# Performance work log

Hardware: AMD Instinct MI355X
Metric: run time of the kernel (lower is better)

Reference implementation:

```python
import jax, jax.numpy as jnp
import numpy as np

B, T, N_STOCKS = 256, 250, 500
HIDDEN, N_LAYERS = 512, 2
LB, UB = 0.0, 0.1
N_ITER = 30  # rebalance fixed-point iterations; extra iters are exact no-ops once converged


def setup_inputs() -> dict:
    key = jax.random.key(0)
    ks = jax.random.split(key, 16)
    s = 1.0 / np.sqrt(HIDDEN)  # torch GRU init scale
    inp = {"x": jax.random.normal(ks[0], (B, T, N_STOCKS), jnp.float32)}
    in_dims = [N_STOCKS, HIDDEN]
    for l in range(N_LAYERS):
        inp[f"w_ih_l{l}"] = jax.random.uniform(ks[1 + 4 * l], (3 * HIDDEN, in_dims[l]), jnp.float32, -s, s)
        inp[f"w_hh_l{l}"] = jax.random.uniform(ks[2 + 4 * l], (3 * HIDDEN, HIDDEN), jnp.float32, -s, s)
        inp[f"b_ih_l{l}"] = jax.random.uniform(ks[3 + 4 * l], (3 * HIDDEN,), jnp.float32, -s, s)
        inp[f"b_hh_l{l}"] = jax.random.uniform(ks[4 + 4 * l], (3 * HIDDEN,), jnp.float32, -s, s)
    inp["fc_w"] = jax.random.uniform(ks[9], (N_STOCKS, HIDDEN), jnp.float32, -s, s)
    inp["fc_b"] = jax.random.uniform(ks[10], (N_STOCKS,), jnp.float32, -s, s)
    return inp


def gru_layer(x, w_ih, w_hh, b_ih, b_hh):
    # x: [B, T, D] -> hidden sequence [B, T, H]; torch gate order: r, z, n
    gi = jnp.einsum('btd,gd->btg', x, w_ih) + b_ih  # precompute input gates [B, T, 3H]

    def cell(h, gi_t):
        gh = h @ w_hh.T + b_hh
        i_r, i_z, i_n = jnp.split(gi_t, 3, axis=-1)
        h_r, h_z, h_n = jnp.split(gh, 3, axis=-1)
        r = jax.nn.sigmoid(i_r + h_r)
        z = jax.nn.sigmoid(i_z + h_z)
        n = jnp.tanh(i_n + r * h_n)
        h_new = (1.0 - z) * n + z * h
        return h_new, h_new

    h0 = jnp.zeros((x.shape[0], HIDDEN), x.dtype)
    _, hs = jax.lax.scan(cell, h0, jnp.swapaxes(gi, 0, 1))  # scan over time
    return jnp.swapaxes(hs, 0, 1)


def rebalance(w):
    # Batched capped-simplex redistribution: clamp to [LB, UB], then push the
    # clipped mass onto non-capped entries proportionally; repeat to fixed point.
    def body(w, _):
        wc = jnp.clip(w, LB, UB)
        leftover = jnp.sum(w - wc, axis=-1, keepdims=True)
        nom = jnp.where(wc != UB, wc, 0.0)
        w_new = wc + leftover * nom / jnp.sum(nom, axis=-1, keepdims=True)
        return w_new, None

    w, _ = jax.lax.scan(body, w, None, length=N_ITER)
    return w


def reference(x, w_ih_l0, w_hh_l0, b_ih_l0, b_hh_l0,
              w_ih_l1, w_hh_l1, b_ih_l1, b_hh_l1, fc_w, fc_b):
    h = gru_layer(x, w_ih_l0, w_hh_l0, b_ih_l0, b_hh_l0)
    h = gru_layer(h, w_ih_l1, w_hh_l1, b_ih_l1, b_hh_l1)
    h_t = h[:, -1, :]                      # last timestep [B, H]
    logit = h_t @ fc_w.T + fc_b            # dropout is identity at inference
    logit = jax.nn.silu(logit)             # swish
    w = jax.nn.softmax(logit, axis=-1)
    return rebalance(w)
```

## Files before the change

### kernel.cpp

```cpp
#include <hip/hip_runtime.h>
#include <math.h>

typedef __attribute__((ext_vector_type(8))) short short8;
typedef __attribute__((ext_vector_type(4))) float floatx4;
typedef unsigned short ushort_t;
typedef unsigned int uint32;
typedef unsigned long long u64;

#define BB 256
#define TT 250
#define NS 500
#define HH 512
#define NBLK 256
#define TBLK 256
#define PL_USH 131072u
#define CH_USH 8192u
#define WHI_USH 32768
#define SCR_OFF 131072
#define SMEMB (131072 + 2 * 32 * 65 * 4)

__device__ __forceinline__ ushort_t f2bf(float f) {
    uint32 u = __float_as_uint(f);
    u += 0x7fffu + ((u >> 16) & 1u);
    return (ushort_t)(u >> 16);
}
__device__ __forceinline__ float bf2f(ushort_t h) { return __uint_as_float(((uint32)h) << 16); }
__device__ __forceinline__ float sigm(float x) { return 1.f / (1.f + expf(-x)); }
__device__ __forceinline__ floatx4 mfma16(short8 a, short8 b, floatx4 c) {
    return __builtin_amdgcn_mfma_f32_16x16x32_bf16(a, b, c, 0, 0, 0);
}
__device__ __forceinline__ u64 pack4(const ushort_t* a) {
    return (u64)a[0] | ((u64)a[1] << 16) | ((u64)a[2] << 32) | ((u64)a[3] << 48);
}
__device__ __forceinline__ void st_agent_u32(ushort_t* p, uint32 v) {
    __hip_atomic_store((uint32*)p, v, __ATOMIC_RELAXED, __HIP_MEMORY_SCOPE_AGENT);
}
__device__ __forceinline__ void st_agent_u64(ushort_t* p, u64 v) {
    __hip_atomic_store((u64*)p, v, __ATOMIC_RELAXED, __HIP_MEMORY_SCOPE_AGENT);
}

__device__ __forceinline__ void dbar(unsigned* flags, unsigned phase, int bid) {
    const int tj = threadIdx.x;
    const unsigned v0 = phase << 1, v1 = (phase << 1) | 1u;
    __syncthreads();
    if (tj == 0)
        __hip_atomic_store(flags + ((size_t)bid << 4), v0,
                           __ATOMIC_RELAXED, __HIP_MEMORY_SCOPE_AGENT);
    if (tj >= 1 && tj < 16) {
        unsigned* sp = flags + ((size_t)((bid - tj) & 255) << 4);
        while (__hip_atomic_load(sp, __ATOMIC_RELAXED, __HIP_MEMORY_SCOPE_AGENT) < v0)
            __builtin_amdgcn_s_sleep(2);
    }
    __syncthreads();
    if (tj == 0)
        __hip_atomic_store(flags + ((size_t)bid << 4), v1,
                           __ATOMIC_RELAXED, __HIP_MEMORY_SCOPE_AGENT);
    if (tj >= 1 && tj < 16) {
        unsigned* sp = flags + ((size_t)((bid - (tj << 4)) & 255) << 4);
        while (__hip_atomic_load(sp, __ATOMIC_RELAXED, __HIP_MEMORY_SCOPE_AGENT) < v1)
            __builtin_amdgcn_s_sleep(2);
    }
    __syncthreads();
}

__device__ __forceinline__ float block_max4(float v, float* scr) {
#pragma unroll
    for (int off = 32; off; off >>= 1) v = fmaxf(v, __shfl_down(v, off, 64));
    if ((threadIdx.x & 63) == 0) scr[threadIdx.x >> 6] = v;
    __syncthreads();
    if (threadIdx.x == 0)
        scr[8] = fmaxf(fmaxf(scr[0], scr[1]), fmaxf(scr[2], scr[3]));
    __syncthreads();
    float r = scr[8];
    __syncthreads();
    return r;
}
__device__ __forceinline__ float2 block_sum2_4(float a, float b, float* scr) {
#pragma unroll
    for (int off = 32; off; off >>= 1) {
        a += __shfl_down(a, off, 64);
        b += __shfl_down(b, off, 64);
    }
    if ((threadIdx.x & 63) == 0) { int w = threadIdx.x >> 6; scr[w] = a; scr[4 + w] = b; }
    __syncthreads();
    if (threadIdx.x == 0) {
        scr[8] = scr[0] + scr[1] + scr[2] + scr[3];
        scr[9] = scr[4] + scr[5] + scr[6] + scr[7];
    }
    __syncthreads();
    float2 r = make_float2(scr[8], scr[9]);
    __syncthreads();
    return r;
}

__device__ __forceinline__ void gemm_both(const ushort_t* __restrict__ gp,
                                          const ushort_t* __restrict__ hp,
                                          const ushort_t* whiS, const ushort_t* wloS,
                                          floatx4 (&aGI)[2][2], floatx4 (&aGH)[2][2]) {
    short8 Bh0[8], Bh1[8], Bl0[8], Bl1[8];
    const ushort_t* gpl = gp + PL_USH;
    const ushort_t* hpl = hp + PL_USH;

#define ISSUE(pc) do {                                                                    \
        const ushort_t* _ph = ((pc) < 16) ? (gp + (size_t)(pc) * CH_USH)                  \
                                          : (hp + (size_t)((pc) - 16) * CH_USH);          \
        const ushort_t* _pl = ((pc) < 16) ? (gpl + (size_t)(pc) * CH_USH)                 \
                                          : (hpl + (size_t)((pc) - 16) * CH_USH);         \
        asm volatile("global_load_dwordx4 %0, %1, off sc0 sc1"                            \
                     : "=v"(Bh0[(pc) & 7]) : "v"(_ph));                                   \
        asm volatile("global_load_dwordx4 %0, %1, off offset:1024 sc0 sc1"                \
                     : "=v"(Bh1[(pc) & 7]) : "v"(_ph));                                   \
        asm volatile("global_load_dwordx4 %0, %1, off sc0 sc1"                            \
                     : "=v"(Bl0[(pc) & 7]) : "v"(_pl));                                   \
        asm volatile("global_load_dwordx4 %0, %1, off offset:1024 sc0 sc1"                \
                     : "=v"(Bl1[(pc) & 7]) : "v"(_pl));                                   \
    } while (0)

    ISSUE(0); ISSUE(1); ISSUE(2); ISSUE(3); ISSUE(4); ISSUE(5); ISSUE(6);

    short8 w0h = *(const short8*)(whiS);
    short8 w1h = *(const short8*)(whiS + 512);
    short8 w0l = *(const short8*)(wloS);
    short8 w1l = *(const short8*)(wloS + 512);

#define GSTEP(c, N) do {                                                                  \
        if ((c) + 7 < 32) ISSUE((c) + 7);                                                 \
        short8 n0h, n1h, n0l, n1l;                                                        \
        if ((c) + 1 < 32) {                                                               \
            const size_t _w = (size_t)(((c) + 1) * 2) * 512;                              \
            n0h = *(const short8*)(whiS + _w);                                            \
            n1h = *(const short8*)(whiS + _w + 512);                                      \
            n0l = *(const short8*)(wloS + _w);                                            \
            n1l = *(const short8*)(wloS + _w + 512);                                      \
        }                                                                                 \
        asm volatile("s_waitcnt vmcnt(" #N ")" ::: "memory");                             \
        __builtin_amdgcn_sched_barrier(0);                                                \
        const int _cs = (c) & 7;                                                          \
        floatx4 (&A)[2][2] = ((c) < 16) ? aGI : aGH;                                      \
        A[0][0] = mfma16(w0h, Bh0[_cs], A[0][0]);                                         \
        A[0][1] = mfma16(w0h, Bh1[_cs], A[0][1]);                                         \
        A[1][0] = mfma16(w1h, Bh0[_cs], A[1][0]);                                         \
        A[1][1] = mfma16(w1h, Bh1[_cs], A[1][1]);                                         \
        A[0][0] = mfma16(w0h, Bl0[_cs], A[0][0]);                                         \
        A[0][1] = mfma16(w0h, Bl1[_cs], A[0][1]);                                         \
        A[1][0] = mfma16(w1h, Bl0[_cs], A[1][0]);                                         \
        A[1][1] = mfma16(w1h, Bl1[_cs], A[1][1]);                                         \
        A[0][0] = mfma16(w0l, Bh0[_cs], A[0][0]);                                         \
        A[0][1] = mfma16(w0l, Bh1[_cs], A[0][1]);                                         \
        A[1][0] = mfma16(w1l, Bh0[_cs], A[1][0]);                                         \
        A[1][1] = mfma16(w1l, Bh1[_cs], A[1][1]);                                         \
        if ((c) + 1 < 32) { w0h = n0h; w1h = n1h; w0l = n0l; w1l = n1l; }                 \
    } while (0)

    GSTEP(0, 28);  GSTEP(1, 28);  GSTEP(2, 28);  GSTEP(3, 28);  GSTEP(4, 28);
    GSTEP(5, 28);  GSTEP(6, 28);  GSTEP(7, 28);  GSTEP(8, 28);  GSTEP(9, 28);
    GSTEP(10, 28); GSTEP(11, 28); GSTEP(12, 28); GSTEP(13, 28); GSTEP(14, 28);
    GSTEP(15, 28); GSTEP(16, 28); GSTEP(17, 28); GSTEP(18, 28); GSTEP(19, 28);
    GSTEP(20, 28); GSTEP(21, 28); GSTEP(22, 28); GSTEP(23, 28); GSTEP(24, 28);
    GSTEP(25, 24); GSTEP(26, 20); GSTEP(27, 16); GSTEP(28, 12); GSTEP(29, 8);
    GSTEP(30, 4);  GSTEP(31, 0);
#undef GSTEP
#undef ISSUE
}

__global__ void __launch_bounds__(TBLK, 1)
gru_main(const float* __restrict__ x,
         const float* __restrict__ wih0, const float* __restrict__ whh0,
         const float* __restrict__ bi0,  const float* __restrict__ bh0,
         const float* __restrict__ wih1, const float* __restrict__ whh1,
         const float* __restrict__ bi1,  const float* __restrict__ bh1,
         const float* __restrict__ fcb,  const float* __restrict__ fcT,
         ushort_t* xpack, ushort_t* h0pack, ushort_t* h1pack,
         unsigned* flags,
         float* __restrict__ out)
{
    extern __shared__ char smem_raw[];
    ushort_t* whi = (ushort_t*)smem_raw;
    ushort_t* wlo = whi + WHI_USH;
    float* scrF = (float*)(smem_raw + SCR_OFF);

    const int bid = blockIdx.x, tid = threadIdx.x;
    const int L  = bid >> 7;
    const int UG = (bid >> 1) & 63;
    const int CT = bid & 1;
    const int wid = tid >> 6, lane = tid & 63;
    const int q = lane >> 4, n = lane & 15;

    {
        const float* Wgi = L ? wih1 : wih0;
        const float* Wgh = L ? whh1 : whh0;
        const int Kgi = L ? HH : NS;
        for (int idx = tid; idx < 32768; idx += TBLK) {
            const int j = idx & 7, ln = (idx >> 3) & 63, rc = idx >> 9;
            const int c = rc >> 1, rt = rc & 1;
            const int m = ln & 15, qq = ln >> 4;
            const int lr = rt * 16 + m;
            const int g = lr >> 3, u = lr & 7;
            float v = 0.f;
            if (g < 3) {
                if (c < 16) {
                    const int k = c * 32 + qq * 8 + j;
                    if (k < Kgi) v = Wgi[(size_t)(g * HH + UG * 8 + u) * Kgi + k];
                } else {
                    const int k = (c - 16) * 32 + qq * 8 + j;
                    v = Wgh[(size_t)(g * HH + UG * 8 + u) * HH + k];
                }
            }
            const ushort_t hb = f2bf(v);
            whi[idx] = hb;
            wlo[idx] = f2bf(v - bf2f(hb));
        }
    }

    const int lb = tid & 63, u2 = (tid >> 6) * 2;
    float biR[2], biZ[2], biN[2], bhR[2], bhZ[2], bhN[2];
    {
        const float* bi = L ? bi1 : bi0;
        const float* bh = L ? bh1 : bh0;
#pragma unroll
        for (int p = 0; p < 2; ++p) {
            const int ugl = UG * 8 + u2 + p;
            biR[p] = bi[ugl]; biZ[p] = bi[HH + ugl]; biN[p] = bi[2 * HH + ugl];
            bhR[p] = bh[ugl]; bhZ[p] = bh[HH + ugl]; bhN[p] = bh[2 * HH + ugl];
        }
    }
    float hreg[4] = {0.f, 0.f, 0.f, 0.f};
    const int chW = UG >> 2, qqW = UG & 3;
    __syncthreads();

    const ushort_t* whiS = whi + (size_t)lane * 8;
    const ushort_t* wloS = wlo + (size_t)lane * 8;
    const size_t apoff = ((size_t)(CT * 8 + wid * 2) * 64 + lane) * 8;

    unsigned phase = 0;
    for (int s = 0; s <= TT; ++s) {
        const bool active = L ? (s >= 1) : (s < TT);
        if (active) {
            const ushort_t *gisrc, *ghsrc;
            if (L == 0) {
                gisrc = xpack + (size_t)(s & 1) * 2 * PL_USH;
                ghsrc = h0pack + (size_t)((s - 1) & 1) * 2 * PL_USH;
            } else {
                gisrc = h0pack + (size_t)((s - 1) & 1) * 2 * PL_USH;
                ghsrc = h1pack + (size_t)(s & 1) * 2 * PL_USH;
            }
            floatx4 z4 = {0.f, 0.f, 0.f, 0.f};
            floatx4 aGI[2][2], aGH[2][2];
#pragma unroll
            for (int i = 0; i < 2; ++i) { aGI[i][0] = z4; aGI[i][1] = z4; aGH[i][0] = z4; aGH[i][1] = z4; }
            gemm_both(gisrc + apoff, ghsrc + apoff, whiS, wloS, aGI, aGH);

            float4 xv0, xv1;
            const bool doX = (s <= TT - 2) && (bid * TBLK + tid < 16384);
            int xko = 0, xb = 0;
            if (doX) {
                const int gx = bid * TBLK + tid;
                xko = gx & 63; xb = gx >> 6;
                const float* xs = x + ((size_t)xb * TT + (s + 1)) * NS + xko * 8;
                if (xko < 62) { xv0 = *(const float4*)(xs); xv1 = *(const float4*)(xs + 4); }
                else {
                    float tmp[8];
#pragma unroll
                    for (int j = 0; j < 8; ++j) {
                        const int k = xko * 8 + j;
                        tmp[j] = (k < NS) ? xs[j] : 0.f;
                    }
                    xv0 = make_float4(tmp[0], tmp[1], tmp[2], tmp[3]);
                    xv1 = make_float4(tmp[4], tmp[5], tmp[6], tmp[7]);
                }
            }

            ushort_t* pk = L ? h1pack + (size_t)((s - 1) & 1) * 2 * PL_USH
                             : h0pack + (size_t)(s & 1) * 2 * PL_USH;
#pragma unroll
            for (int h = 0; h < 2; ++h) {
                if ((wid >> 1) == h) {
#pragma unroll
                    for (int rt = 0; rt < 2; ++rt)
#pragma unroll
                        for (int t = 0; t < 2; ++t) {
                            const int row0 = rt * 16 + q * 4;
                            const int colr = ((wid & 1) * 2 + t) * 16 + n;
#pragma unroll
                            for (int r4 = 0; r4 < 4; ++r4) {
                                scrF[(row0 + r4) * 65 + colr] = aGI[rt][t][r4];
                                scrF[2080 + (row0 + r4) * 65 + colr] = aGH[rt][t][r4];
                            }
                        }
                }
                __syncthreads();
                float hvv[2];
#pragma unroll
                for (int p = 0; p < 2; ++p) {
                    const int u = u2 + p;
                    const float gir = scrF[u * 65 + lb],        ghr = scrF[2080 + u * 65 + lb];
                    const float giz = scrF[(8 + u) * 65 + lb],  ghz = scrF[2080 + (8 + u) * 65 + lb];
                    const float gin = scrF[(16 + u) * 65 + lb], ghn = scrF[2080 + (16 + u) * 65 + lb];
                    const float rr = sigm(gir + biR[p] + ghr + bhR[p]);
                    const float zz = sigm(giz + biZ[p] + ghz + bhZ[p]);
                    const float nn = tanhf(gin + biN[p] + rr * (ghn + bhN[p]));
                    const float hv = (1.f - zz) * nn + zz * hreg[h * 2 + p];
                    hreg[h * 2 + p] = hv;
                    hvv[p] = hv;
                }
                {
                    const int b = CT * 128 + h * 64 + lb;
                    const size_t o8 = ((size_t)(chW * 16 + (b >> 4)) * 64 + qqW * 16 + (b & 15)) * 8;
                    const ushort_t hb0 = f2bf(hvv[0]), hb1 = f2bf(hvv[1]);
                    const uint32 hi2 = (uint32)hb0 | ((uint32)hb1 << 16);
                    const uint32 lo2 = (uint32)f2bf(hvv[0] - bf2f(hb0)) |
                                       ((uint32)f2bf(hvv[1] - bf2f(hb1)) << 16);
                    st_agent_u32(pk + o8 + u2, hi2);
                    st_agent_u32(pk + PL_USH + o8 + u2, lo2);
                }
                __syncthreads();
            }

            if (doX) {
                ushort_t hi8[8], lo8[8];
                float vv[8] = {xv0.x, xv0.y, xv0.z, xv0.w, xv1.x, xv1.y, xv1.z, xv1.w};
#pragma unroll
                for (int j = 0; j < 8; ++j) {
                    hi8[j] = f2bf(vv[j]);
                    lo8[j] = f2bf(vv[j] - bf2f(hi8[j]));
                }
                ushort_t* xp = xpack + (size_t)((s + 1) & 1) * 2 * PL_USH;
                const size_t o = ((size_t)((xko >> 2) * 16 + (xb >> 4)) * 64 + (xko & 3) * 16 + (xb & 15)) * 8;
                st_agent_u64(xp + o, pack4(hi8));
                st_agent_u64(xp + o + 4, pack4(hi8 + 4));
                st_agent_u64(xp + PL_USH + o, pack4(lo8));
                st_agent_u64(xp + PL_USH + o + 4, pack4(lo8 + 4));
            }
        } else if ((s <= TT - 2) && (bid * TBLK + tid < 16384)) {
            const int gx = bid * TBLK + tid;
            const int xko = gx & 63, xb = gx >> 6;
            const float* xs = x + ((size_t)xb * TT + (s + 1)) * NS + xko * 8;
            ushort_t hi8[8], lo8[8];
#pragma unroll
            for (int j = 0; j < 8; ++j) {
                const int k = xko * 8 + j;
                const float v = (k < NS) ? xs[j] : 0.f;
                hi8[j] = f2bf(v);
                lo8[j] = f2bf(v - bf2f(hi8[j]));
            }
            ushort_t* xp = xpack + (size_t)((s + 1) & 1) * 2 * PL_USH;
            const size_t o = ((size_t)((xko >> 2) * 16 + (xb >> 4)) * 64 + (xko & 3) * 16 + (xb & 15)) * 8;
            st_agent_u64(xp + o, pack4(hi8));
            st_agent_u64(xp + o + 4, pack4(hi8 + 4));
            st_agent_u64(xp + PL_USH + o, pack4(lo8));
            st_agent_u64(xp + PL_USH + o + 4, pack4(lo8 + 4));
        }
        ++phase;
        dbar(flags, phase, bid);
    }

    {
        const int b = bid;
        float* sh = (float*)smem_raw;
        float* scr = sh + 576;
        const ushort_t* pk = h1pack + (size_t)1 * 2 * PL_USH;
        for (int u = tid; u < HH; u += TBLK) {
            const int uo = u >> 3, j = u & 7;
            const size_t o = ((size_t)((uo >> 2) * 16 + (b >> 4)) * 64 + (uo & 3) * 16 + (b & 15)) * 8 + j;
            sh[u] = bf2f(pk[o]) + bf2f(pk[PL_USH + o]);
        }
        __syncthreads();

        const int o1 = tid;
        const bool v2 = (tid + 256) < NS;
        const int o2 = v2 ? (tid + 256) : (NS - 1);
        float a0 = fcb[o1], a1 = fcb[o2];
        for (int k = 0; k < HH; ++k) {
            const float hv = sh[k];
            const float* fr = fcT + (size_t)k * NS;
            a0 = fmaf(hv, fr[o1], a0);
            a1 = fmaf(hv, fr[o2], a1);
        }
        float l0 = a0 * sigm(a0);
        float l1 = a1 * sigm(a1);
        float mx = block_max4(fmaxf(l0, v2 ? l1 : -3.4e38f), scr);
        float e0 = expf(l0 - mx);
        float e1 = v2 ? expf(l1 - mx) : 0.f;
        float2 s2 = block_sum2_4(e0 + e1, 0.f, scr);
        float w0 = e0 / s2.x, w1 = e1 / s2.x;
        for (int it = 0; it < 30; ++it) {
            float c0v = fminf(fmaxf(w0, 0.f), 0.1f);
            float c1v = fminf(fmaxf(w1, 0.f), 0.1f);
            float lv = (w0 - c0v) + (w1 - c1v);
            float n0 = (c0v != 0.1f) ? c0v : 0.f;
            float n1 = (v2 && c1v != 0.1f) ? c1v : 0.f;
            float2 rs = block_sum2_4(lv, n0 + n1, scr);
            float inv = rs.x / rs.y;
            w0 = c0v + inv * n0;
            w1 = c1v + inv * n1;
        }
        out[(size_t)b * NS + o1] = w0;
        if (v2) out[(size_t)b * NS + tid + 256] = w1;
    }
}

__global__ void pack_x0(const float* __restrict__ x, ushort_t* __restrict__ xpack) {
    const int t = blockIdx.x * 256 + threadIdx.x;
    const int ko = t & 63, b = t >> 6;
    const float* xs = x + (size_t)b * TT * NS;
    ushort_t hi8[8], lo8[8];
#pragma unroll
    for (int j = 0; j < 8; ++j) {
        const int k = ko * 8 + j;
        const float v = (k < NS) ? xs[k] : 0.f;
        hi8[j] = f2bf(v);
        lo8[j] = f2bf(v - bf2f(hi8[j]));
    }
    const size_t o = ((size_t)((ko >> 2) * 16 + (b >> 4)) * 64 + (ko & 3) * 16 + (b & 15)) * 8;
    *(uint4*)(xpack + o) = *(uint4*)hi8;
    *(uint4*)(xpack + PL_USH + o) = *(uint4*)lo8;
}

__global__ void transpose_k(const float* __restrict__ src, float* __restrict__ dst,
                            int G, int K) {
    int idx = blockIdx.x * 256 + threadIdx.x;
    if (idx >= G * K) return;
    int k = idx / G, g = idx - k * G;
    dst[idx] = src[(size_t)g * K + k];
}

extern "C" void kernel_launch(void* const* d_in, const int* in_sizes, int n_in,
                              void* d_out, int out_size, void* d_ws, size_t ws_size,
                              hipStream_t stream) {
    const float* x    = (const float*)d_in[0];
    const float* wih0 = (const float*)d_in[1];
    const float* whh0 = (const float*)d_in[2];
    const float* bih0 = (const float*)d_in[3];
    const float* bhh0 = (const float*)d_in[4];
    const float* wih1 = (const float*)d_in[5];
    const float* whh1 = (const float*)d_in[6];
    const float* bih1 = (const float*)d_in[7];
    const float* bhh1 = (const float*)d_in[8];
    const float* fcw  = (const float*)d_in[9];
    const float* fcb  = (const float*)d_in[10];
    float* outp = (float*)d_out;

    char* ws = (char*)d_ws;
    unsigned* flags  = (unsigned*)ws;
    ushort_t* h0pack = (ushort_t*)(ws + 196608);
    ushort_t* h1pack = (ushort_t*)(ws + 196608 + 1048576);
    ushort_t* xpack  = (ushort_t*)(ws + 196608 + 2097152);
    float*    fcT    = (float*)(ws + 196608 + 3145728);

    hipMemsetAsync(ws, 0, 196608 + 2097152, stream);
    pack_x0<<<64, 256, 0, stream>>>(x, xpack);
    {
        int nel = NS * HH;
        transpose_k<<<(nel + 255) / 256, 256, 0, stream>>>(fcw, fcT, NS, HH);
    }

    hipFuncSetAttribute((const void*)gru_main,
                        hipFuncAttributeMaxDynamicSharedMemorySize, SMEMB);

    void* args[] = {(void*)&x,
                    (void*)&wih0, (void*)&whh0, (void*)&bih0, (void*)&bhh0,
                    (void*)&wih1, (void*)&whh1, (void*)&bih1, (void*)&bhh1,
                    (void*)&fcb, (void*)&fcT,
                    (void*)&xpack, (void*)&h0pack, (void*)&h1pack,
                    (void*)&flags, (void*)&outp};
    hipError_t e = hipLaunchCooperativeKernel((const void*)gru_main, dim3(NBLK), dim3(TBLK),
                                              args, SMEMB, stream);
    if (e != hipSuccess) {
        gru_main<<<dim3(NBLK), dim3(TBLK), SMEMB, stream>>>(
            x, wih0, whh0, bih0, bhh0, wih1, whh1, bih1, bhh1,
            fcb, fcT, xpack, h0pack, h1pack, flags, outp);
    }
}
```

Measured before the change: 3.330 ms.

## Use per-XCD leader cache invalidation in grid barrier and relax load coherence

The GEMM loads of the packed state drop the sc1 bit, so they can hit in the XCD-local L2 instead of going coherent to memory. To keep that correct, the grid barrier gains a step where one elected leader block per XCD runs an agent-scope acquire fence (L2 invalidate) and publishes a per-XCD flag that the other blocks on that XCD spin on. The thread-to-(batch, unit) mapping in the gate epilogue also changes. This adds an extra barrier stage and relies on XCC_ID-based leader election being correct.

```diff
diff --git a/kernel.cpp b/kernel.cpp
--- a/kernel.cpp
+++ b/kernel.cpp
@@ -39,9 +39,11 @@
     __hip_atomic_store((u64*)p, v, __ATOMIC_RELAXED, __HIP_MEMORY_SCOPE_AGENT);
 }
 
-__device__ __forceinline__ void dbar(unsigned* flags, unsigned phase, int bid) {
+__device__ __forceinline__ void dbar(unsigned* flags, unsigned phase, int bid,
+                                     int myxcd, bool isLead) {
     const int tj = threadIdx.x;
     const unsigned v0 = phase << 1, v1 = (phase << 1) | 1u;
+    unsigned* xflags = flags + 4096;
     __syncthreads();
     if (tj == 0)
         __hip_atomic_store(flags + ((size_t)bid << 4), v0,
@@ -61,6 +63,18 @@
             __builtin_amdgcn_s_sleep(2);
     }
     __syncthreads();
+    if (isLead) {
+        if (tj == 0) {
+            __builtin_amdgcn_fence(__ATOMIC_ACQUIRE, "agent");
+            __hip_atomic_store(xflags + ((size_t)myxcd << 4), phase,
+                               __ATOMIC_RELAXED, __HIP_MEMORY_SCOPE_AGENT);
+        }
+    } else if (tj == 0) {
+        unsigned* sp = xflags + ((size_t)myxcd << 4);
+        while (__hip_atomic_load(sp, __ATOMIC_RELAXED, __HIP_MEMORY_SCOPE_AGENT) < phase)
+            __builtin_amdgcn_s_sleep(2);
+    }
+    __syncthreads();
 }
 
 __device__ __forceinline__ float block_max4(float v, float* scr) {
@@ -106,13 +120,13 @@
                                           : (hp + (size_t)((pc) - 16) * CH_USH);          \
         const ushort_t* _pl = ((pc) < 16) ? (gpl + (size_t)(pc) * CH_USH)                 \
                                           : (hpl + (size_t)((pc) - 16) * CH_USH);         \
-        asm volatile("global_load_dwordx4 %0, %1, off sc0 sc1"                            \
+        asm volatile("global_load_dwordx4 %0, %1, off sc0"                                \
                      : "=v"(Bh0[(pc) & 7]) : "v"(_ph));                                   \
-        asm volatile("global_load_dwordx4 %0, %1, off offset:1024 sc0 sc1"                \
+        asm volatile("global_load_dwordx4 %0, %1, off offset:1024 sc0"                    \
                      : "=v"(Bh1[(pc) & 7]) : "v"(_ph));                                   \
-        asm volatile("global_load_dwordx4 %0, %1, off sc0 sc1"                            \
+        asm volatile("global_load_dwordx4 %0, %1, off sc0"                                \
                      : "=v"(Bl0[(pc) & 7]) : "v"(_pl));                                   \
-        asm volatile("global_load_dwordx4 %0, %1, off offset:1024 sc0 sc1"                \
+        asm volatile("global_load_dwordx4 %0, %1, off offset:1024 sc0"                    \
                      : "=v"(Bl1[(pc) & 7]) : "v"(_pl));                                   \
     } while (0)
 
@@ -212,7 +226,18 @@
         }
     }
 
-    const int lb = tid & 63, u2 = (tid >> 6) * 2;
+    int myxcd;
+    asm volatile("s_getreg_b32 %0, hwreg(HW_REG_XCC_ID)" : "=s"(myxcd));
+    myxcd &= 7;
+    if (tid == 0) {
+        unsigned old = atomicCAS(flags + 8192 + ((size_t)myxcd << 4), 0u, (unsigned)bid + 1u);
+        scrF[0] = (old == 0u) ? 1.f : 0.f;
+    }
+    __syncthreads();
+    const bool isLead = (scrF[0] != 0.f);
+
+    const int u2 = (tid & 3) * 2;
+    const int lb = wid * 16 + ((tid & 63) >> 2);
     float biR[2], biZ[2], biN[2], bhR[2], bhZ[2], bhN[2];
     {
         const float* bi = L ? bi1 : bi0;
@@ -351,7 +376,7 @@
             st_agent_u64(xp + PL_USH + o + 4, pack4(lo8 + 4));
         }
         ++phase;
-        dbar(flags, phase, bid);
+        dbar(flags, phase, bid, myxcd, isLead);
     }
 
     {
```

Result: slower. 3.466 ms (+4.1%).

## Flatten grid barrier, deepen load prefetch, and compute gates in registers via shuffles

Applied to the files above, without the earlier changes.

Replaces the two-stage 16-way butterfly grid barrier with a single-stage barrier in which every thread polls one block's flag. Raises the global-load prefetch depth in the fused GEMM from 7 to 11 chunks, with adjusted waitcnt values. Drops the LDS scratch transpose for the gate epilogue: z-gate values are exchanged with cross-lane shuffles, and half the lanes compute the GRU update directly from MFMA accumulators. This removes two block syncs per half and the LDS round trip, at the cost of more register pressure and more concurrent polling traffic on the flags.

```diff
diff --git a/kernel.cpp b/kernel.cpp
--- a/kernel.cpp
+++ b/kernel.cpp
@@ -16,8 +16,7 @@
 #define PL_USH 131072u
 #define CH_USH 8192u
 #define WHI_USH 32768
-#define SCR_OFF 131072
-#define SMEMB (131072 + 2 * 32 * 65 * 4)
+#define SMEMB 131072
 
 __device__ __forceinline__ ushort_t f2bf(float f) {
     uint32 u = __float_as_uint(f);
@@ -40,26 +39,13 @@
 }
 
 __device__ __forceinline__ void dbar(unsigned* flags, unsigned phase, int bid) {
-    const int tj = threadIdx.x;
-    const unsigned v0 = phase << 1, v1 = (phase << 1) | 1u;
-    __syncthreads();
-    if (tj == 0)
-        __hip_atomic_store(flags + ((size_t)bid << 4), v0,
+    __syncthreads();
+    if (threadIdx.x == 0)
+        __hip_atomic_store(flags + ((size_t)bid << 4), phase,
                            __ATOMIC_RELAXED, __HIP_MEMORY_SCOPE_AGENT);
-    if (tj >= 1 && tj < 16) {
-        unsigned* sp = flags + ((size_t)((bid - tj) & 255) << 4);
-        while (__hip_atomic_load(sp, __ATOMIC_RELAXED, __HIP_MEMORY_SCOPE_AGENT) < v0)
-            __builtin_amdgcn_s_sleep(2);
-    }
-    __syncthreads();
-    if (tj == 0)
-        __hip_atomic_store(flags + ((size_t)bid << 4), v1,
-                           __ATOMIC_RELAXED, __HIP_MEMORY_SCOPE_AGENT);
-    if (tj >= 1 && tj < 16) {
-        unsigned* sp = flags + ((size_t)((bid - (tj << 4)) & 255) << 4);
-        while (__hip_atomic_load(sp, __ATOMIC_RELAXED, __HIP_MEMORY_SCOPE_AGENT) < v1)
-            __builtin_amdgcn_s_sleep(2);
-    }
+    unsigned* sp = flags + ((size_t)threadIdx.x << 4);
+    while (__hip_atomic_load(sp, __ATOMIC_RELAXED, __HIP_MEMORY_SCOPE_AGENT) < phase)
+        __builtin_amdgcn_s_sleep(2);
     __syncthreads();
 }
 
@@ -97,7 +83,7 @@
                                           const ushort_t* __restrict__ hp,
                                           const ushort_t* whiS, const ushort_t* wloS,
                                           floatx4 (&aGI)[2][2], floatx4 (&aGH)[2][2]) {
-    short8 Bh0[8], Bh1[8], Bl0[8], Bl1[8];
+    short8 Bh0[12], Bh1[12], Bl0[12], Bl1[12];
     const ushort_t* gpl = gp + PL_USH;
     const ushort_t* hpl = hp + PL_USH;
 
@@ -107,16 +93,17 @@
         const ushort_t* _pl = ((pc) < 16) ? (gpl + (size_t)(pc) * CH_USH)                 \
                                           : (hpl + (size_t)((pc) - 16) * CH_USH);         \
         asm volatile("global_load_dwordx4 %0, %1, off sc0 sc1"                            \
-                     : "=v"(Bh0[(pc) & 7]) : "v"(_ph));                                   \
+                     : "=v"(Bh0[(pc) % 12]) : "v"(_ph));                                  \
         asm volatile("global_load_dwordx4 %0, %1, off offset:1024 sc0 sc1"                \
-                     : "=v"(Bh1[(pc) & 7]) : "v"(_ph));                                   \
+                     : "=v"(Bh1[(pc) % 12]) : "v"(_ph));                                  \
         asm volatile("global_load_dwordx4 %0, %1, off sc0 sc1"                            \
-                     : "=v"(Bl0[(pc) & 7]) : "v"(_pl));                                   \
+                     : "=v"(Bl0[(pc) % 12]) : "v"(_pl));                                  \
         asm volatile("global_load_dwordx4 %0, %1, off offset:1024 sc0 sc1"                \
-                     : "=v"(Bl1[(pc) & 7]) : "v"(_pl));                                   \
+                     : "=v"(Bl1[(pc) % 12]) : "v"(_pl));                                  \
     } while (0)
 
-    ISSUE(0); ISSUE(1); ISSUE(2); ISSUE(3); ISSUE(4); ISSUE(5); ISSUE(6);
+    ISSUE(0); ISSUE(1); ISSUE(2); ISSUE(3); ISSUE(4); ISSUE(5);
+    ISSUE(6); ISSUE(7); ISSUE(8); ISSUE(9); ISSUE(10);
 
     short8 w0h = *(const short8*)(whiS);
     short8 w1h = *(const short8*)(whiS + 512);
@@ -124,7 +111,7 @@
     short8 w1l = *(const short8*)(wloS + 512);
 
 #define GSTEP(c, N) do {                                                                  \
-        if ((c) + 7 < 32) ISSUE((c) + 7);                                                 \
+        if ((c) + 11 < 32) ISSUE((c) + 11);                                               \
         short8 n0h, n1h, n0l, n1l;                                                        \
         if ((c) + 1 < 32) {                                                               \
             const size_t _w = (size_t)(((c) + 1) * 2) * 512;                              \
@@ -135,7 +122,7 @@
         }                                                                                 \
         asm volatile("s_waitcnt vmcnt(" #N ")" ::: "memory");                             \
         __builtin_amdgcn_sched_barrier(0);                                                \
-        const int _cs = (c) & 7;                                                          \
+        const int _cs = (c) % 12;                                                         \
         floatx4 (&A)[2][2] = ((c) < 16) ? aGI : aGH;                                      \
         A[0][0] = mfma16(w0h, Bh0[_cs], A[0][0]);                                         \
         A[0][1] = mfma16(w0h, Bh1[_cs], A[0][1]);                                         \
@@ -152,11 +139,11 @@
         if ((c) + 1 < 32) { w0h = n0h; w1h = n1h; w0l = n0l; w1l = n1l; }                 \
     } while (0)
 
-    GSTEP(0, 28);  GSTEP(1, 28);  GSTEP(2, 28);  GSTEP(3, 28);  GSTEP(4, 28);
-    GSTEP(5, 28);  GSTEP(6, 28);  GSTEP(7, 28);  GSTEP(8, 28);  GSTEP(9, 28);
-    GSTEP(10, 28); GSTEP(11, 28); GSTEP(12, 28); GSTEP(13, 28); GSTEP(14, 28);
-    GSTEP(15, 28); GSTEP(16, 28); GSTEP(17, 28); GSTEP(18, 28); GSTEP(19, 28);
-    GSTEP(20, 28); GSTEP(21, 28); GSTEP(22, 28); GSTEP(23, 28); GSTEP(24, 28);
+    GSTEP(0, 44);  GSTEP(1, 44);  GSTEP(2, 44);  GSTEP(3, 44);  GSTEP(4, 44);
+    GSTEP(5, 44);  GSTEP(6, 44);  GSTEP(7, 44);  GSTEP(8, 44);  GSTEP(9, 44);
+    GSTEP(10, 44); GSTEP(11, 44); GSTEP(12, 44); GSTEP(13, 44); GSTEP(14, 44);
+    GSTEP(15, 44); GSTEP(16, 44); GSTEP(17, 44); GSTEP(18, 44); GSTEP(19, 44);
+    GSTEP(20, 44); GSTEP(21, 40); GSTEP(22, 36); GSTEP(23, 32); GSTEP(24, 28);
     GSTEP(25, 24); GSTEP(26, 20); GSTEP(27, 16); GSTEP(28, 12); GSTEP(29, 8);
     GSTEP(30, 4);  GSTEP(31, 0);
 #undef GSTEP
@@ -177,14 +164,12 @@
     extern __shared__ char smem_raw[];
     ushort_t* whi = (ushort_t*)smem_raw;
     ushort_t* wlo = whi + WHI_USH;
-    float* scrF = (float*)(smem_raw + SCR_OFF);
 
     const int bid = blockIdx.x, tid = threadIdx.x;
     const int L  = bid >> 7;
     const int UG = (bid >> 1) & 63;
     const int CT = bid & 1;
     const int wid = tid >> 6, lane = tid & 63;
-    const int q = lane >> 4, n = lane & 15;
 
     {
         const float* Wgi = L ? wih1 : wih0;
@@ -212,19 +197,19 @@
         }
     }
 
-    const int lb = tid & 63, u2 = (tid >> 6) * 2;
-    float biR[2], biZ[2], biN[2], bhR[2], bhZ[2], bhN[2];
+    const int ub = ((lane >> 4) & 1) * 4;
+    float biR[4], biZ[4], biN[4], bhR[4], bhZ[4], bhN[4];
     {
         const float* bi = L ? bi1 : bi0;
         const float* bh = L ? bh1 : bh0;
 #pragma unroll
-        for (int p = 0; p < 2; ++p) {
-            const int ugl = UG * 8 + u2 + p;
+        for (int p = 0; p < 4; ++p) {
+            const int ugl = UG * 8 + ub + p;
             biR[p] = bi[ugl]; biZ[p] = bi[HH + ugl]; biN[p] = bi[2 * HH + ugl];
             bhR[p] = bh[ugl]; bhZ[p] = bh[HH + ugl]; bhN[p] = bh[2 * HH + ugl];
         }
     }
-    float hreg[4] = {0.f, 0.f, 0.f, 0.f};
+    float hreg[2][4] = {{0.f, 0.f, 0.f, 0.f}, {0.f, 0.f, 0.f, 0.f}};
     const int chW = UG >> 2, qqW = UG & 3;
     __syncthreads();
 
@@ -270,50 +255,40 @@
                 }
             }
 
+            float zGI[2][4], zGH[2][4];
+#pragma unroll
+            for (int t = 0; t < 2; ++t)
+#pragma unroll
+                for (int r = 0; r < 4; ++r) {
+                    zGI[t][r] = __shfl_xor(aGI[0][t][r], 32, 64);
+                    zGH[t][r] = __shfl_xor(aGH[0][t][r], 32, 64);
+                }
             ushort_t* pk = L ? h1pack + (size_t)((s - 1) & 1) * 2 * PL_USH
                              : h0pack + (size_t)(s & 1) * 2 * PL_USH;
-#pragma unroll
-            for (int h = 0; h < 2; ++h) {
-                if ((wid >> 1) == h) {
-#pragma unroll
-                    for (int rt = 0; rt < 2; ++rt)
-#pragma unroll
-                        for (int t = 0; t < 2; ++t) {
-                            const int row0 = rt * 16 + q * 4;
-                            const int colr = ((wid & 1) * 2 + t) * 16 + n;
-#pragma unroll
-                            for (int r4 = 0; r4 < 4; ++r4) {
-                                scrF[(row0 + r4) * 65 + colr] = aGI[rt][t][r4];
-                                scrF[2080 + (row0 + r4) * 65 + colr] = aGH[rt][t][r4];
-                            }
-                        }
+            if (lane < 32) {
+#pragma unroll
+                for (int t = 0; t < 2; ++t) {
+                    ushort_t hi4[4], lo4[4];
+#pragma unroll
+                    for (int r = 0; r < 4; ++r) {
+                        const float gir = aGI[0][t][r], ghr = aGH[0][t][r];
+                        const float giz = zGI[t][r],    ghz = zGH[t][r];
+                        const float gin = aGI[1][t][r], ghn = aGH[1][t][r];
+                        const float rr = sigm(gir + biR[r] + ghr + bhR[r]);
+                        const float zz = sigm(giz + biZ[r] + ghz + bhZ[r]);
+                        const float nn = tanhf(gin + biN[r] + rr * (ghn + bhN[r]));
+                        const float hv = (1.f - zz) * nn + zz * hreg[t][r];
+                        hreg[t][r] = hv;
+                        hi4[r] = f2bf(hv);
+                        lo4[r] = f2bf(hv - bf2f(hi4[r]));
+                    }
+                    const int b = CT * 128 + wid * 32 + t * 16 + (lane & 15);
+                    const size_t o8 = ((size_t)(chW * 16 + (b >> 4)) * 64 + qqW * 16 + (b & 15)) * 8 + ub;
+                    st_agent_u32(pk + o8,     (uint32)hi4[0] | ((uint32)hi4[1] << 16));
+                    st_agent_u32(pk + o8 + 2, (uint32)hi4[2] | ((uint32)hi4[3] << 16));
+                    st_agent_u32(pk + PL_USH + o8,     (uint32)lo4[0] | ((uint32)lo4[1] << 16));
+                    st_agent_u32(pk + PL_USH + o8 + 2, (uint32)lo4[2] | ((uint32)lo4[3] << 16));
                 }
-                __syncthreads();
-                float hvv[2];
-#pragma unroll
-                for (int p = 0; p < 2; ++p) {
-                    const int u = u2 + p;
-                    const float gir = scrF[u * 65 + lb],        ghr = scrF[2080 + u * 65 + lb];
-                    const float giz = scrF[(8 + u) * 65 + lb],  ghz = scrF[2080 + (8 + u) * 65 + lb];
-                    const float gin = scrF[(16 + u) * 65 + lb], ghn = scrF[2080 + (16 + u) * 65 + lb];
-                    const float rr = sigm(gir + biR[p] + ghr + bhR[p]);
-                    const float zz = sigm(giz + biZ[p] + ghz + bhZ[p]);
-                    const float nn = tanhf(gin + biN[p] + rr * (ghn + bhN[p]));
-                    const float hv = (1.f - zz) * nn + zz * hreg[h * 2 + p];
-                    hreg[h * 2 + p] = hv;
-                    hvv[p] = hv;
-                }
-                {
-                    const int b = CT * 128 + h * 64 + lb;
-                    const size_t o8 = ((size_t)(chW * 16 + (b >> 4)) * 64 + qqW * 16 + (b & 15)) * 8;
-                    const ushort_t hb0 = f2bf(hvv[0]), hb1 = f2bf(hvv[1]);
-                    const uint32 hi2 = (uint32)hb0 | ((uint32)hb1 << 16);
-                    const uint32 lo2 = (uint32)f2bf(hvv[0] - bf2f(hb0)) |
-                                       ((uint32)f2bf(hvv[1] - bf2f(hb1)) << 16);
-                    st_agent_u32(pk + o8 + u2, hi2);
-                    st_agent_u32(pk + PL_USH + o8 + u2, lo2);
-                }
-                __syncthreads();
             }
 
             if (doX) {
```

Result: no change. 3.342 ms (+0.4%).
